# Kernel tuning notes

Measured on AMD Instinct MI355X. Metric: run time of the kernel, lower is better.

## Reference

```python
import jax, jax.numpy as jnp
import numpy as np

B, T, D = 2, 4096, 2048
H, K = 16, 128          # num_heads, head_dim (V == K)
P = H * K               # projection size
C = 64                  # chunk_size
CONV = 4                # conv_size
LAT = 128               # snapshot_latent_dim
CPS = 256 // C          # chunks_per_snapshot
EPS = 1e-6


def _silu(x):
    return x * jax.nn.sigmoid(x)


def _dwconv_silu(x, w):
    # causal depthwise conv1d: x (B,T,P), w (P,CONV)
    y = jax.lax.conv_general_dilated(
        x.transpose(0, 2, 1), w[:, None, :], (1,), [(w.shape[-1] - 1, 0)],
        feature_group_count=x.shape[-1], dimension_numbers=('NCH', 'OIH', 'NCH'))
    return _silu(y.transpose(0, 2, 1))


def _rmsnorm(x, w, eps=EPS):
    return x * jax.lax.rsqrt(jnp.mean(x * x, axis=-1, keepdims=True) + eps) * w


def _l2norm(x):
    return x * jax.lax.rsqrt(jnp.sum(x * x, axis=-1, keepdims=True) + 1e-12)


def setup_inputs() -> dict:
    key = jax.random.key(0)
    ks = jax.random.split(key, 20)
    sD, sK = D ** -0.5, K ** -0.5
    return {
        'x': jax.random.normal(ks[0], (B, T, D), jnp.float32),
        'Wq': jax.random.normal(ks[1], (P, D), jnp.float32) * sD,
        'Wk': jax.random.normal(ks[2], (P, D), jnp.float32) * sD,
        'Wv': jax.random.normal(ks[3], (P, D), jnp.float32) * sD,
        'conv_q': jax.random.normal(ks[4], (P, CONV), jnp.float32) * 0.5,
        'conv_k': jax.random.normal(ks[5], (P, CONV), jnp.float32) * 0.5,
        'conv_v': jax.random.normal(ks[6], (P, CONV), jnp.float32) * 0.5,
        'A_log': jnp.log(jax.random.uniform(ks[7], (H,), jnp.float32, 1.0, 8.0)),
        'dt_bias': jax.random.normal(ks[8], (P,), jnp.float32) * 0.1 - 3.0,
        'Wfa': jax.random.normal(ks[9], (K, D), jnp.float32) * sD,
        'Wfb': jax.random.normal(ks[10], (P, K), jnp.float32) * sK,
        'Wb': jax.random.normal(ks[11], (H, D), jnp.float32) * sD,
        'Wga': jax.random.normal(ks[12], (K, D), jnp.float32) * sD,
        'Wgb': jax.random.normal(ks[13], (P, K), jnp.float32) * sK,
        'bgb': jnp.zeros((P,), jnp.float32),
        'o_norm_w': jnp.ones((K,), jnp.float32),
        'Wo': jax.random.normal(ks[14], (D, P), jnp.float32) * (P ** -0.5),
        'snap_norm_w': jnp.ones((K * K,), jnp.float32),
        'snap_down': jax.random.normal(ks[15], (LAT, K * K), jnp.float32) * (K ** -1.0),
    }


def _forward(x, Wq, Wk, Wv, conv_q, conv_k, conv_v, A_log, dt_bias, Wfa, Wfb,
             Wb, Wga, Wgb, bgb, o_norm_w, Wo, snap_norm_w, snap_down):
    Bx, Tx, _ = x.shape
    Nc = Tx // C
    # projections + short causal conv + silu
    q = _dwconv_silu(x @ Wq.T, conv_q).reshape(Bx, Tx, H, K)
    k = _dwconv_silu(x @ Wk.T, conv_k).reshape(Bx, Tx, H, K)
    v = _dwconv_silu(x @ Wv.T, conv_v).reshape(Bx, Tx, H, K)
    # KDA gate: log forget gate per (t, h, k)
    g_raw = (x @ Wfa.T) @ Wfb.T                               # (B,T,P)
    log_g = (-jnp.exp(A_log))[None, None, :, None] * \
        jax.nn.softplus(g_raw + dt_bias).reshape(Bx, Tx, H, K)
    beta = jax.nn.sigmoid(x @ Wb.T)                           # (B,T,H)
    # qk l2-norm + scale
    q = _l2norm(q) * (K ** -0.5)
    k = _l2norm(k)
    # chunk: (B,T,H,K) -> (B,H,Nc,C,K)
    def ch(a):
        return a.reshape(Bx, Nc, C, H, -1).transpose(0, 3, 1, 2, 4)
    qc, kc, vc, gc = ch(q), ch(k), ch(v), ch(log_g)
    bc = beta.reshape(Bx, Nc, C, H).transpose(0, 3, 1, 2)     # (B,H,Nc,C)
    cum = jnp.maximum(jnp.cumsum(gc, axis=-2), -15.0)
    Wg = jnp.exp(cum)
    Wi = jnp.exp(-cum)
    u_mat = kc * Wi
    w_mat = kc * Wg
    q_tilde = qc * Wg
    be = bc[..., None]
    bw = be * w_mat
    bv = be * vc
    L = jnp.tril(jnp.einsum('bhnik,bhnjk->bhnij', bw, u_mat), -1)
    A_mat = L + jnp.eye(C, dtype=L.dtype)
    ev = jax.lax.linalg.triangular_solve(A_mat, bv, left_side=True, lower=True, unit_diagonal=True)
    ew = jax.lax.linalg.triangular_solve(A_mat, bw, left_side=True, lower=True, unit_diagonal=True)
    intra = jnp.tril(jnp.einsum('bhnik,bhnjk->bhnij', q_tilde, u_mat), 0)
    w_last = Wg[..., -1, :]                                   # (B,H,Nc,K)

    def body(S, inp):
        qt_n, um_n, ev_n, ew_n, ia_n, wl_n = inp
        delta = ev_n - ew_n @ S                               # (B,H,C,V)
        o_n = qt_n @ S + ia_n @ delta
        S_new = wl_n[..., None] * (S + jnp.einsum('bhck,bhcv->bhkv', um_n, delta))
        return S_new, (o_n, S_new)

    xs = tuple(jnp.moveaxis(a, 2, 0) for a in (q_tilde, u_mat, ev, ew, intra, w_last))
    S0 = jnp.zeros((Bx, H, K, K), jnp.float32)
    _, (o_chunks, S_all) = jax.lax.scan(body, S0, xs)
    out = o_chunks.transpose(1, 0, 3, 2, 4).reshape(Bx, Tx, H, K)
    # compressed snapshots every CPS chunks
    S_snap = S_all[CPS - 1::CPS]                              # (Ns,B,H,K,K)
    Ns = S_snap.shape[0]
    flat = S_snap.reshape(Ns, Bx, H, K * K)
    snaps = (_rmsnorm(flat, snap_norm_w) @ snap_down.T).transpose(1, 0, 2, 3)  # (B,Ns,H,LAT)
    # gated output norm + output projection
    gate = ((x @ Wga.T) @ Wgb.T + bgb).reshape(Bx, Tx, H, K)
    o = _rmsnorm(out, o_norm_w) * jax.nn.sigmoid(gate)
    y = o.reshape(Bx, Tx, P) @ Wo.T
    return y, snaps


def reference(x, Wq, Wk, Wv, conv_q, conv_k, conv_v, A_log, dt_bias, Wfa, Wfb,
              Wb, Wga, Wgb, bgb, o_norm_w, Wo, snap_norm_w, snap_down):
    return _forward(x, Wq, Wk, Wv, conv_q, conv_k, conv_v, A_log, dt_bias,
                    Wfa, Wfb, Wb, Wga, Wgb, bgb, o_norm_w, Wo,
                    snap_norm_w, snap_down)
```

## Files before the change

kernel.cpp:

```cpp
#include <hip/hip_runtime.h>

constexpr int Bc   = 2;
constexpr int Tc   = 4096;
constexpr int Dc   = 2048;
constexpr int Hc   = 16;
constexpr int Kc   = 128;
constexpr int Pc   = Hc * Kc;
constexpr int Cc   = 64;
constexpr int NCc  = Tc / Cc;
constexpr int Mc   = Bc * Tc;
constexpr int LATc = 128;

__device__ __forceinline__ float bf2f(unsigned short u) {
  unsigned int x = ((unsigned int)u) << 16;
  return __builtin_bit_cast(float, x);
}
__device__ __forceinline__ unsigned short f2bf(float f) {
  unsigned int x = __builtin_bit_cast(unsigned int, f);
  x += 0x7fffu + ((x >> 16) & 1u);
  return (unsigned short)(x >> 16);
}
__device__ __forceinline__ float4 ld4(const float* p) {
  return *reinterpret_cast<const float4*>(p);
}
__device__ __forceinline__ float4 ld4(const unsigned short* p) {
  ushort4 u = *reinterpret_cast<const ushort4*>(p);
  return make_float4(bf2f(u.x), bf2f(u.y), bf2f(u.z), bf2f(u.w));
}
__device__ __forceinline__ void st1(float* p, float v) { *p = v; }
__device__ __forceinline__ void st1(unsigned short* p, float v) { *p = f2bf(v); }

__device__ __forceinline__ float fsig(float x) {
  return __fdividef(1.f, 1.f + __expf(-x));
}
__device__ __forceinline__ float fsoftplus(float g) {
  return (g > 20.f) ? g : __logf(1.f + __expf(g));
}

typedef __attribute__((ext_vector_type(8))) short bf16x8;
typedef __attribute__((ext_vector_type(4))) float f32x4;

__device__ __forceinline__ int swzA(int row, int kbyte) { return row * 256 + (kbyte ^ ((row & 7) << 4)); }
__device__ __forceinline__ int swzB(int row, int kbyte) { return row * 128 + (kbyte ^ ((row & 7) << 4)); }
__device__ __forceinline__ bf16x8 ldsv8(const unsigned short* base, int byteoff) {
  return *reinterpret_cast<const bf16x8*>(reinterpret_cast<const char*>(base) + byteoff);
}
__device__ __forceinline__ void stsv16B(unsigned short* base, int byteoff, int4 v) {
  *reinterpret_cast<int4*>(reinterpret_cast<char*>(base) + byteoff) = v;
}
__device__ __forceinline__ void stsv8B(unsigned short* base, int byteoff, uint2 v) {
  *reinterpret_cast<uint2*>(reinterpret_cast<char*>(base) + byteoff) = v;
}
__device__ __forceinline__ unsigned short lds16(const unsigned short* base, int byteoff) {
  return *reinterpret_cast<const unsigned short*>(reinterpret_cast<const char*>(base) + byteoff);
}

__device__ __forceinline__ int xcd_swz(int id, int nwg) {
  if ((nwg & 7) != 0 || nwg < 16) return id;
  return (id & 7) * (nwg >> 3) + (id >> 3);
}

__global__ void cast_f32_bf16(const float* __restrict__ in, unsigned short* __restrict__ out,
                              int n) {
  int i = (blockIdx.x * 256 + threadIdx.x) * 4;
  if (i < n) {
    float4 v = ld4(in + i);
    ushort4 o;
    o.x = f2bf(v.x); o.y = f2bf(v.y); o.z = f2bf(v.z); o.w = f2bf(v.w);
    *reinterpret_cast<ushort4*>(out + i) = o;
  }
}

__device__ __forceinline__ void gload_lds16(const unsigned short* g, unsigned short* l) {
  __builtin_amdgcn_global_load_lds(
      (const __attribute__((address_space(1))) void*)g,
      (__attribute__((address_space(3))) void*)l, 16, 0, 0);
}

__device__ __forceinline__ void tile_map(int& m0, int& n0) {
  int id = blockIdx.y * gridDim.x + blockIdx.x;
  id = xcd_swz(id, gridDim.x * gridDim.y);
  const int bpg = gridDim.y << 3;
  int grp = id / bpg, rem = id % bpg;
  m0 = ((grp << 3) + (rem & 7)) * 128;
  n0 = (rem >> 3) * 128;
}

template <typename OT>
__global__ __launch_bounds__(256) void gemm_nt_mfma(const unsigned short* __restrict__ A,
                                                    const unsigned short* __restrict__ Bm,
                                                    OT* __restrict__ Out,
                                                    int Ndim, int Kd) {
  __shared__ __align__(16) unsigned short As[128 * 32];
  __shared__ __align__(16) unsigned short Bs[128 * 32];
  int m0, n0;
  tile_map(m0, n0);
  const int tid = threadIdx.x;
  const int wave = tid >> 6;
  const int lane = tid & 63;
  const int wr = wave >> 1, wc = wave & 1;
  const int l15 = lane & 15, l4 = lane >> 4;
  const int kxor = (l4 ^ ((l15 >> 1) & 3)) << 3;
  f32x4 acc[4][4] = {};

  for (int k0 = 0; k0 < Kd; k0 += 32) {
#pragma unroll
    for (int i = 0; i < 2; ++i) {
      int slot = (wave * 2 + i) * 64 + lane;
      int r = slot >> 2;
      int kg = (slot & 3) ^ ((r >> 1) & 3);
      gload_lds16(&A[(size_t)(m0 + r) * Kd + k0 + kg * 8], &As[(wave * 2 + i) * 512]);
      gload_lds16(&Bm[(size_t)(n0 + r) * Kd + k0 + kg * 8], &Bs[(wave * 2 + i) * 512]);
    }
    __syncthreads();
    bf16x8 af[4], bfr[4];
#pragma unroll
    for (int m = 0; m < 4; ++m)
      af[m] = *reinterpret_cast<const bf16x8*>(&As[(wr * 64 + m * 16 + l15) * 32 + kxor]);
#pragma unroll
    for (int n = 0; n < 4; ++n)
      bfr[n] = *reinterpret_cast<const bf16x8*>(&Bs[(wc * 64 + n * 16 + l15) * 32 + kxor]);
#pragma unroll
    for (int m = 0; m < 4; ++m)
#pragma unroll
      for (int n = 0; n < 4; ++n)
        acc[m][n] = __builtin_amdgcn_mfma_f32_16x16x32_bf16(af[m], bfr[n], acc[m][n], 0, 0, 0);
    __syncthreads();
  }
#pragma unroll
  for (int m = 0; m < 4; ++m)
#pragma unroll
    for (int n = 0; n < 4; ++n)
#pragma unroll
      for (int r = 0; r < 4; ++r) {
        int row = m0 + wr * 64 + m * 16 + l4 * 4 + r;
        int col = n0 + wc * 64 + n * 16 + l15;
        st1(&Out[(size_t)row * Ndim + col], acc[m][n][r]);
      }
}

__global__ __launch_bounds__(256) void gemm_nt_mfma_qkv(const unsigned short* __restrict__ A,
                                                        const unsigned short* __restrict__ Bm,
                                                        unsigned short* __restrict__ Out,
                                                        int Kd) {
  __shared__ __align__(16) unsigned short As[128 * 32];
  __shared__ __align__(16) unsigned short Bs[128 * 32];
  int m0, n0;
  tile_map(m0, n0);
  const int tid = threadIdx.x;
  const int wave = tid >> 6;
  const int lane = tid & 63;
  const int wr = wave >> 1, wc = wave & 1;
  const int l15 = lane & 15, l4 = lane >> 4;
  const int kxor = (l4 ^ ((l15 >> 1) & 3)) << 3;
  f32x4 acc[4][4] = {};

  for (int k0 = 0; k0 < Kd; k0 += 32) {
#pragma unroll
    for (int i = 0; i < 2; ++i) {
      int slot = (wave * 2 + i) * 64 + lane;
      int r = slot >> 2;
      int kg = (slot & 3) ^ ((r >> 1) & 3);
      gload_lds16(&A[(size_t)(m0 + r) * Kd + k0 + kg * 8], &As[(wave * 2 + i) * 512]);
      gload_lds16(&Bm[(size_t)(n0 + r) * Kd + k0 + kg * 8], &Bs[(wave * 2 + i) * 512]);
    }
    __syncthreads();
    bf16x8 af[4], bfr[4];
#pragma unroll
    for (int m = 0; m < 4; ++m)
      af[m] = *reinterpret_cast<const bf16x8*>(&As[(wr * 64 + m * 16 + l15) * 32 + kxor]);
#pragma unroll
    for (int n = 0; n < 4; ++n)
      bfr[n] = *reinterpret_cast<const bf16x8*>(&Bs[(wc * 64 + n * 16 + l15) * 32 + kxor]);
#pragma unroll
    for (int m = 0; m < 4; ++m)
#pragma unroll
      for (int n = 0; n < 4; ++n)
        acc[m][n] = __builtin_amdgcn_mfma_f32_16x16x32_bf16(af[m], bfr[n], acc[m][n], 0, 0, 0);
    __syncthreads();
  }
  unsigned short* dst = Out + (size_t)(n0 >> 11) * ((size_t)Mc * 2048);
  const int cbase = n0 & 2047;
#pragma unroll
  for (int m = 0; m < 4; ++m)
#pragma unroll
    for (int n = 0; n < 4; ++n)
#pragma unroll
      for (int r = 0; r < 4; ++r) {
        int row = m0 + wr * 64 + m * 16 + l4 * 4 + r;
        int col = cbase + wc * 64 + n * 16 + l15;
        dst[(size_t)row * 2048 + col] = f2bf(acc[m][n][r]);
      }
}

__global__ __launch_bounds__(256) void gemm_nt_mfma_sk(const unsigned short* __restrict__ A,
                                                       const unsigned short* __restrict__ Bm,
                                                       float* __restrict__ Part,
                                                       int Ndim, int Kd, int kslice, int Mtot) {
  __shared__ __align__(16) unsigned short As[128 * 32];
  __shared__ __align__(16) unsigned short Bs[128 * 32];
  const int m0 = blockIdx.x * 128;
  const int n0 = blockIdx.y * 128;
  const int kz = blockIdx.z * kslice;
  const int tid = threadIdx.x;
  const int wave = tid >> 6;
  const int lane = tid & 63;
  const int wr = wave >> 1, wc = wave & 1;
  const int l15 = lane & 15, l4 = lane >> 4;
  const int kxor = (l4 ^ ((l15 >> 1) & 3)) << 3;
  f32x4 acc[4][4] = {};

  for (int k0 = kz; k0 < kz + kslice; k0 += 32) {
#pragma unroll
    for (int i = 0; i < 2; ++i) {
      int slot = (wave * 2 + i) * 64 + lane;
      int r = slot >> 2;
      int kg = (slot & 3) ^ ((r >> 1) & 3);
      gload_lds16(&A[(size_t)(m0 + r) * Kd + k0 + kg * 8], &As[(wave * 2 + i) * 512]);
      gload_lds16(&Bm[(size_t)(n0 + r) * Kd + k0 + kg * 8], &Bs[(wave * 2 + i) * 512]);
    }
    __syncthreads();
    bf16x8 af[4], bfr[4];
#pragma unroll
    for (int m = 0; m < 4; ++m)
      af[m] = *reinterpret_cast<const bf16x8*>(&As[(wr * 64 + m * 16 + l15) * 32 + kxor]);
#pragma unroll
    for (int n = 0; n < 4; ++n)
      bfr[n] = *reinterpret_cast<const bf16x8*>(&Bs[(wc * 64 + n * 16 + l15) * 32 + kxor]);
#pragma unroll
    for (int m = 0; m < 4; ++m)
#pragma unroll
      for (int n = 0; n < 4; ++n)
        acc[m][n] = __builtin_amdgcn_mfma_f32_16x16x32_bf16(af[m], bfr[n], acc[m][n], 0, 0, 0);
    __syncthreads();
  }
  float* out = Part + (size_t)blockIdx.z * Mtot * Ndim;
#pragma unroll
  for (int m = 0; m < 4; ++m)
#pragma unroll
    for (int n = 0; n < 4; ++n)
#pragma unroll
      for (int r = 0; r < 4; ++r) {
        int row = m0 + wr * 64 + m * 16 + l4 * 4 + r;
        int col = n0 + wc * 64 + n * 16 + l15;
        out[(size_t)row * Ndim + col] = acc[m][n][r];
      }
}

__global__ __launch_bounds__(256) void chunk_prep(
    const unsigned short* __restrict__ q_lin, const unsigned short* __restrict__ k_lin,
    const unsigned short* __restrict__ v_lin, const unsigned short* __restrict__ g_raw,
    const float* __restrict__ beta_lin, const float* __restrict__ conv_q,
    const float* __restrict__ conv_k, const float* __restrict__ conv_v,
    const float* __restrict__ A_log, const float* __restrict__ dt_bias,
    unsigned short* __restrict__ qt, unsigned short* __restrict__ u_,
    unsigned short* __restrict__ bv, unsigned short* __restrict__ bw,
    float* __restrict__ wlast) {
  const int wave = threadIdx.x >> 6, lane = threadIdx.x & 63;
  const int cid = blockIdx.x * 4 + wave;
  const int n = cid & 63;
  const int h = (cid >> 6) & 15;
  const int b = cid >> 10;
  const int k0 = 2 * lane;
  const int p = h * Kc + k0;
  float cq[2][4], ck[2][4], cv[2][4];
#pragma unroll
  for (int s = 0; s < 2; ++s)
#pragma unroll
    for (int j = 0; j < 4; ++j) {
      cq[s][j] = conv_q[(p + s) * 4 + j];
      ck[s][j] = conv_k[(p + s) * 4 + j];
      cv[s][j] = conv_v[(p + s) * 4 + j];
    }
  const float aneg = -__expf(A_log[h]);
  const float db0 = dt_bias[p], db1 = dt_bias[p + 1];
  float cum0 = 0.f, cum1 = 0.f;
  const int t0 = n * Cc;
  float wq[2][3] = {}, wk[2][3] = {}, wv[2][3] = {};
#pragma unroll
  for (int d = 0; d < 3; ++d) {
    int ts = t0 - 3 + d;
    if (ts >= 0) {
      size_t o = ((size_t)(b * Tc + ts)) * Pc + p;
      ushort2 q2 = *(const ushort2*)(q_lin + o);
      ushort2 k2 = *(const ushort2*)(k_lin + o);
      ushort2 v2 = *(const ushort2*)(v_lin + o);
      wq[0][d] = bf2f(q2.x); wq[1][d] = bf2f(q2.y);
      wk[0][d] = bf2f(k2.x); wk[1][d] = bf2f(k2.y);
      wv[0][d] = bf2f(v2.x); wv[1][d] = bf2f(v2.y);
    }
  }
  for (int c = 0; c < Cc; ++c) {
    const int t = t0 + c;
    size_t off = ((size_t)(b * Tc + t)) * Pc + p;
    ushort2 q2 = *(const ushort2*)(q_lin + off);
    ushort2 k2 = *(const ushort2*)(k_lin + off);
    ushort2 v2 = *(const ushort2*)(v_lin + off);
    ushort2 g2 = *(const ushort2*)(g_raw + off);
    float nq[2] = {bf2f(q2.x), bf2f(q2.y)};
    float nk[2] = {bf2f(k2.x), bf2f(k2.y)};
    float nv[2] = {bf2f(v2.x), bf2f(v2.y)};
    float qv[2], kv[2], vv[2];
#pragma unroll
    for (int s = 0; s < 2; ++s) {
      qv[s] = cq[s][0] * wq[s][0] + cq[s][1] * wq[s][1] + cq[s][2] * wq[s][2] + cq[s][3] * nq[s];
      kv[s] = ck[s][0] * wk[s][0] + ck[s][1] * wk[s][1] + ck[s][2] * wk[s][2] + ck[s][3] * nk[s];
      vv[s] = cv[s][0] * wv[s][0] + cv[s][1] * wv[s][1] + cv[s][2] * wv[s][2] + cv[s][3] * nv[s];
      wq[s][0] = wq[s][1]; wq[s][1] = wq[s][2]; wq[s][2] = nq[s];
      wk[s][0] = wk[s][1]; wk[s][1] = wk[s][2]; wk[s][2] = nk[s];
      wv[s][0] = wv[s][1]; wv[s][1] = wv[s][2]; wv[s][2] = nv[s];
      qv[s] = qv[s] * fsig(qv[s]);
      kv[s] = kv[s] * fsig(kv[s]);
      vv[s] = vv[s] * fsig(vv[s]);
    }
    float a = qv[0] * qv[0] + qv[1] * qv[1];
    float bb = kv[0] * kv[0] + kv[1] * kv[1];
#pragma unroll
    for (int off2 = 32; off2 > 0; off2 >>= 1) {
      a += __shfl_xor(a, off2, 64);
      bb += __shfl_xor(bb, off2, 64);
    }
    float rq = rsqrtf(a + 1e-12f) * 0.08838834764831845f;
    float rk = rsqrtf(bb + 1e-12f);
    float g0 = bf2f(g2.x) + db0, g1 = bf2f(g2.y) + db1;
    cum0 += aneg * fsoftplus(g0);
    cum1 += aneg * fsoftplus(g1);
    float cc0 = fmaxf(cum0, -15.f), cc1 = fmaxf(cum1, -15.f);
    float Wg0 = __expf(cc0), Wg1 = __expf(cc1);
    float Wi0 = __fdividef(1.f, Wg0), Wi1 = __fdividef(1.f, Wg1);
    float beta = fsig(beta_lin[((size_t)(b * Tc + t)) * 128 + h]);
    size_t idx = ((size_t)cid * Cc + c) * Kc + k0;
    ushort2 o1, o2, o3, o4;
    o1.x = f2bf(qv[0] * rq * Wg0); o1.y = f2bf(qv[1] * rq * Wg1);
    o2.x = f2bf(kv[0] * rk * Wi0); o2.y = f2bf(kv[1] * rk * Wi1);
    o3.x = f2bf(beta * kv[0] * rk * Wg0); o3.y = f2bf(beta * kv[1] * rk * Wg1);
    o4.x = f2bf(beta * vv[0]); o4.y = f2bf(beta * vv[1]);
    *(ushort2*)(qt + idx) = o1;
    *(ushort2*)(u_ + idx) = o2;
    *(ushort2*)(bw + idx) = o3;
    *(ushort2*)(bv + idx) = o4;
    if (c == Cc - 1) {
      wlast[(size_t)cid * Kc + k0] = Wg0;
      wlast[(size_t)cid * Kc + k0 + 1] = Wg1;
    }
  }
}

__global__ __launch_bounds__(256) void chunk_solve_mfma(
    const unsigned short* __restrict__ qt, unsigned short* __restrict__ u_,
    unsigned short* __restrict__ evb,
    unsigned short* __restrict__ ewb,
    unsigned short* __restrict__ intra_out) {
  const int blk = blockIdx.x;
  const size_t base = (size_t)blk * (Cc * Kc);
  const size_t ibase = (size_t)blk * (Cc * Cc);
  const int tid = threadIdx.x, wave = tid >> 6, lane = tid & 63;
  const int l15 = lane & 15, l4 = lane >> 4;

  __shared__ __align__(16) char lds[65536];
  unsigned short* uS   = (unsigned short*)(lds);
  unsigned short* qtS  = (unsigned short*)(lds + 16384);
  unsigned short* bwS  = (unsigned short*)(lds + 32768);
  unsigned short* NLrm = (unsigned short*)(lds + 49152);
  unsigned short* NLT  = (unsigned short*)(lds + 57344);
  unsigned short* Trm  = (unsigned short*)(lds);
  unsigned short* TT   = (unsigned short*)(lds + 8192);
  unsigned short* Prm  = (unsigned short*)(lds + 16384);
  unsigned short* PT   = (unsigned short*)(lds + 24576);
  unsigned short* bvT  = (unsigned short*)(lds + 32768);
  unsigned short* bwT  = (unsigned short*)(lds + 49152);

#pragma unroll
  for (int i = 0; i < 4; ++i) {
    int cid = tid + i * 256;
    int r = cid >> 4, c8 = (cid & 15) * 8, cb2 = (cid & 15) * 16;
    int4 vu = *(const int4*)(u_ + base + (size_t)r * 128 + c8);
    int4 vb = *(const int4*)(ewb + base + (size_t)r * 128 + c8);
    int4 vq = *(const int4*)(qt + base + (size_t)r * 128 + c8);
    stsv16B(uS, swzA(r, cb2), vu);
    stsv16B(bwS, swzA(r, cb2), vb);
    stsv16B(qtS, swzA(r, cb2), vq);
  }
  __syncthreads();

  const int arow = 16 * wave + l15;
  bf16x8 aBw[4], aQt[4];
#pragma unroll
  for (int ks = 0; ks < 4; ++ks) {
    aBw[ks] = ldsv8(bwS, swzA(arow, 16 * l4 + 64 * ks));
    aQt[ks] = ldsv8(qtS, swzA(arow, 16 * l4 + 64 * ks));
  }
  f32x4 Lc[4], Ic[4];
#pragma unroll
  for (int nt = 0; nt < 4; ++nt) {
    f32x4 a = {}, bq = {};
#pragma unroll
    for (int ks = 0; ks < 4; ++ks) {
      bf16x8 bu = ldsv8(uS, swzA(16 * nt + l15, 16 * l4 + 64 * ks));
      a = __builtin_amdgcn_mfma_f32_16x16x32_bf16(aBw[ks], bu, a, 0, 0, 0);
      bq = __builtin_amdgcn_mfma_f32_16x16x32_bf16(aQt[ks], bu, bq, 0, 0, 0);
    }
    Lc[nt] = a; Ic[nt] = bq;
  }
#pragma unroll
  for (int nt = 0; nt < 4; ++nt)
#pragma unroll
    for (int r = 0; r < 4; ++r) {
      int row = 16 * wave + 4 * l4 + r, col = 16 * nt + l15;
      intra_out[ibase + (size_t)row * 64 + col] = f2bf((col <= row) ? Ic[nt][r] : 0.f);
    }

#pragma unroll
  for (int i = 0; i < 4; ++i) {
    int w2 = tid + i * 256;
    int k = w2 >> 3, cg = w2 & 7;
    unsigned short tmp[8];
#pragma unroll
    for (int j = 0; j < 8; ++j) {
      int c = cg + 8 * j;
      tmp[j] = lds16(uS, swzA(c, 2 * k));
    }
#pragma unroll
    for (int j = 0; j < 8; ++j)
      u_[base + (size_t)k * 64 + cg + 8 * j] = tmp[j];
  }
  __syncthreads();

  f32x4 Tf[4];
#pragma unroll
  for (int nt = 0; nt < 4; ++nt)
#pragma unroll
    for (int r = 0; r < 4; ++r) {
      int row = 16 * wave + 4 * l4 + r, col = 16 * nt + l15;
      float nl = (col < row) ? -Lc[nt][r] : 0.f;
      unsigned short nb = f2bf(nl);
      *reinterpret_cast<unsigned short*>((char*)NLrm + swzB(row, col * 2)) = nb;
      *reinterpret_cast<unsigned short*>((char*)NLT + swzB(col, row * 2)) = nb;
      float t0 = nl + ((row == col) ? 1.f : 0.f);
      Tf[nt][r] = t0;
      unsigned short tb = f2bf(t0);
      *reinterpret_cast<unsigned short*>((char*)Trm + swzB(row, col * 2)) = tb;
      *reinterpret_cast<unsigned short*>((char*)TT + swzB(col, row * 2)) = tb;
    }
  __syncthreads();

  bf16x8 aN[2];
#pragma unroll
  for (int ks = 0; ks < 2; ++ks) aN[ks] = ldsv8(NLrm, swzB(arow, 16 * l4 + 64 * ks));
  f32x4 Pf[4];
#pragma unroll
  for (int nt = 0; nt < 4; ++nt) {
    f32x4 acc = {};
#pragma unroll
    for (int ks = 0; ks < 2; ++ks)
      acc = __builtin_amdgcn_mfma_f32_16x16x32_bf16(aN[ks], ldsv8(NLT, swzB(16 * nt + l15, 16 * l4 + 64 * ks)), acc, 0, 0, 0);
    Pf[nt] = acc;
  }
  int4 rv[4], rw[4];
#pragma unroll
  for (int i = 0; i < 4; ++i) {
    int cid = tid + i * 256;
    int r = cid >> 4, c8 = (cid & 15) * 8;
    rv[i] = *(const int4*)(evb + base + (size_t)r * 128 + c8);
    rw[i] = *(const int4*)(ewb + base + (size_t)r * 128 + c8);
  }
#pragma unroll
  for (int nt = 0; nt < 4; ++nt)
#pragma unroll
    for (int r = 0; r < 4; ++r) {
      int row = 16 * wave + 4 * l4 + r, col = 16 * nt + l15;
      unsigned short pb = f2bf(Pf[nt][r]);
      *reinterpret_cast<unsigned short*>((char*)Prm + swzB(row, col * 2)) = pb;
      *reinterpret_cast<unsigned short*>((char*)PT + swzB(col, row * 2)) = pb;
    }
  __syncthreads();

  for (int it = 0; it < 5; ++it) {
    bf16x8 aP[2];
#pragma unroll
    for (int ks = 0; ks < 2; ++ks) aP[ks] = ldsv8(Prm, swzB(arow, 16 * l4 + 64 * ks));
    f32x4 Tn[4], Pn[4];
#pragma unroll
    for (int nt = 0; nt < 4; ++nt) {
      f32x4 acc = Tf[nt];
#pragma unroll
      for (int ks = 0; ks < 2; ++ks)
        acc = __builtin_amdgcn_mfma_f32_16x16x32_bf16(aP[ks], ldsv8(TT, swzB(16 * nt + l15, 16 * l4 + 64 * ks)), acc, 0, 0, 0);
      Tn[nt] = acc;
    }
    if (it < 4) {
#pragma unroll
      for (int nt = 0; nt < 4; ++nt) {
        f32x4 acc = {};
#pragma unroll
        for (int ks = 0; ks < 2; ++ks)
          acc = __builtin_amdgcn_mfma_f32_16x16x32_bf16(aP[ks], ldsv8(PT, swzB(16 * nt + l15, 16 * l4 + 64 * ks)), acc, 0, 0, 0);
        Pn[nt] = acc;
      }
    }
    __syncthreads();
#pragma unroll
    for (int nt = 0; nt < 4; ++nt)
#pragma unroll
      for (int r = 0; r < 4; ++r) {
        int row = 16 * wave + 4 * l4 + r, col = 16 * nt + l15;
        unsigned short tb = f2bf(Tn[nt][r]);
        *reinterpret_cast<unsigned short*>((char*)Trm + swzB(row, col * 2)) = tb;
        *reinterpret_cast<unsigned short*>((char*)TT + swzB(col, row * 2)) = tb;
        if (it < 4) {
          unsigned short pb = f2bf(Pn[nt][r]);
          *reinterpret_cast<unsigned short*>((char*)Prm + swzB(row, col * 2)) = pb;
          *reinterpret_cast<unsigned short*>((char*)PT + swzB(col, row * 2)) = pb;
        }
      }
#pragma unroll
    for (int nt = 0; nt < 4; ++nt) Tf[nt] = Tn[nt];
    __syncthreads();
  }

#pragma unroll
  for (int i = 0; i < 4; ++i) {
    int cid = tid + i * 256;
    int r = cid >> 4;
    const unsigned short* pv = reinterpret_cast<const unsigned short*>(&rv[i]);
    const unsigned short* pw = reinterpret_cast<const unsigned short*>(&rw[i]);
#pragma unroll
    for (int j = 0; j < 8; ++j) {
      int v = (cid & 15) * 8 + j;
      *reinterpret_cast<unsigned short*>((char*)bvT + swzB(v, r * 2)) = pv[j];
      *reinterpret_cast<unsigned short*>((char*)bwT + swzB(v, r * 2)) = pw[j];
    }
  }
  __syncthreads();

  bf16x8 aT[2];
#pragma unroll
  for (int ks = 0; ks < 2; ++ks) aT[ks] = ldsv8(Trm, swzB(arow, 16 * l4 + 64 * ks));
#pragma unroll
  for (int nt = 0; nt < 8; ++nt) {
    f32x4 e = {}, w2 = {};
#pragma unroll
    for (int ks = 0; ks < 2; ++ks) {
      e = __builtin_amdgcn_mfma_f32_16x16x32_bf16(aT[ks], ldsv8(bvT, swzB(16 * nt + l15, 16 * l4 + 64 * ks)), e, 0, 0, 0);
      w2 = __builtin_amdgcn_mfma_f32_16x16x32_bf16(aT[ks], ldsv8(bwT, swzB(16 * nt + l15, 16 * l4 + 64 * ks)), w2, 0, 0, 0);
    }
#pragma unroll
    for (int r = 0; r < 4; ++r) {
      int row = 16 * wave + 4 * l4 + r, col = 16 * nt + l15;
      evb[base + (size_t)row * 128 + col] = f2bf(e[r]);
      ewb[base + (size_t)row * 128 + col] = f2bf(w2[r]);
    }
  }
}

__global__ __launch_bounds__(512) void scan_mfma(
    const unsigned short* __restrict__ qt, const unsigned short* __restrict__ uT,
    const unsigned short* __restrict__ evb, const unsigned short* __restrict__ ewb,
    const unsigned short* __restrict__ intra, const float* __restrict__ wlast,
    unsigned short* __restrict__ attn_o, unsigned short* __restrict__ snapb) {
  const int blk = blockIdx.x;
  const int bh = blk >> 1, vh = blk & 1;
  const int b = bh >> 4, h = bh & 15;
  const int v0 = vh * 64;
  const int tid = threadIdx.x, wave = tid >> 6, lane = tid & 63;
  const int l15 = lane & 15, l4 = lane >> 4;
  __shared__ __align__(16) unsigned short ewS[8192];
  __shared__ __align__(16) unsigned short qtS[8192];
  __shared__ __align__(16) unsigned short uTS[8192];
  __shared__ __align__(16) unsigned short iaS[4096];
  __shared__ __align__(16) unsigned short evS[4096];
  __shared__ __align__(16) unsigned short sBT[8192];
  __shared__ __align__(16) unsigned short dBT[4096];

  f32x4 S[4] = {};
  {
    int4 z = {0, 0, 0, 0};
    stsv16B(sBT, tid * 32, z);
    stsv16B(sBT, tid * 32 + 16, z);
  }

  const int sr = tid >> 3;
  const int sk0 = (tid & 7) * 16;
  const int sc0 = (tid & 7) * 8;
  const int tk = tid >> 3;
  const int wloff = 16 * wave + 4 * l4;
  int4 rEw0, rEw1, rQt0, rQt1, rEv, rUT0, rUT1, rIa;
  float4 rWlN, rWlC;

#define STAGE_LOAD(CB, IB, NN)                                                    \
  rEw0 = *(const int4*)(ewb + (CB) + sr * 128 + sk0);                             \
  rEw1 = *(const int4*)(ewb + (CB) + sr * 128 + sk0 + 8);                         \
  rQt0 = *(const int4*)(qt + (CB) + sr * 128 + sk0);                              \
  rQt1 = *(const int4*)(qt + (CB) + sr * 128 + sk0 + 8);                          \
  rEv = *(const int4*)(evb + (CB) + sr * 128 + v0 + sc0);                         \
  rUT0 = *(const int4*)(uT + (CB) + (size_t)tk * 64 + sc0);                       \
  rUT1 = *(const int4*)(uT + (CB) + (size_t)(tk + 64) * 64 + sc0);                \
  rIa = *(const int4*)(intra + (IB) + sr * 64 + sc0);                             \
  rWlN = ld4(wlast + ((size_t)bh * 64 + (NN)) * 128 + wloff);

#define STAGE_WRITE()                                                             \
  stsv16B(ewS, swzA(sr, sk0 * 2), rEw0);                                          \
  stsv16B(ewS, swzA(sr, sk0 * 2 + 16), rEw1);                                     \
  stsv16B(qtS, swzA(sr, sk0 * 2), rQt0);                                          \
  stsv16B(qtS, swzA(sr, sk0 * 2 + 16), rQt1);                                     \
  stsv16B(evS, swzB(sr, sc0 * 2), rEv);                                           \
  stsv16B(iaS, swzB(sr, sc0 * 2), rIa);                                           \
  stsv16B(uTS, swzB(tk, sc0 * 2), rUT0);                                          \
  stsv16B(uTS, swzB(tk + 64, sc0 * 2), rUT1);

  {
    const size_t cb0 = (size_t)bh * 64 * 8192;
    const size_t ib0 = (size_t)bh * 64 * 4096;
    STAGE_LOAD(cb0, ib0, 0);
    STAGE_WRITE();
    rWlC = rWlN;
  }
  __syncthreads();

  const int m = wave & 3, ntb = (wave >> 2) * 2;
  const int arow = 16 * m + l15;
  const int krow = 16 * wave + l15;

  for (int n = 0; n < NCc; ++n) {
    const size_t cb = ((size_t)bh * 64 + n) * 8192;
    const size_t ib = ((size_t)bh * 64 + n) * 4096;
    if (n < 63) { STAGE_LOAD(cb + 8192, ib + 4096, n + 1); }
    bf16x8 aEw[4];
#pragma unroll
    for (int ks = 0; ks < 4; ++ks) aEw[ks] = ldsv8(ewS, swzA(arow, 16 * l4 + 64 * ks));
#pragma unroll
    for (int i = 0; i < 2; ++i) {
      int vl = 16 * (ntb + i) + l15;
      f32x4 p = {};
#pragma unroll
      for (int ks = 0; ks < 4; ++ks)
        p = __builtin_amdgcn_mfma_f32_16x16x32_bf16(aEw[ks], ldsv8(sBT, swzA(vl, 16 * l4 + 64 * ks)), p, 0, 0, 0);
      float d[4];
#pragma unroll
      for (int r = 0; r < 4; ++r) {
        int c = 16 * m + 4 * l4 + r;
        d[r] = bf2f(lds16(evS, swzB(c, 2 * vl))) - p[r];
      }
      uint2 pk;
      pk.x = (unsigned)f2bf(d[0]) | ((unsigned)f2bf(d[1]) << 16);
      pk.y = (unsigned)f2bf(d[2]) | ((unsigned)f2bf(d[3]) << 16);
      stsv8B(dBT, swzB(vl, (16 * m + 4 * l4) * 2), pk);
    }
    __syncthreads();
    bf16x8 aQt[4], aIa[2], aU[2];
#pragma unroll
    for (int ks = 0; ks < 4; ++ks) aQt[ks] = ldsv8(qtS, swzA(arow, 16 * l4 + 64 * ks));
#pragma unroll
    for (int ks = 0; ks < 2; ++ks) aIa[ks] = ldsv8(iaS, swzB(arow, 16 * l4 + 64 * ks));
#pragma unroll
    for (int ks = 0; ks < 2; ++ks) aU[ks] = ldsv8(uTS, swzB(krow, 16 * l4 + 64 * ks));
#pragma unroll
    for (int i = 0; i < 2; ++i) {
      int vl = 16 * (ntb + i) + l15;
      f32x4 o = {};
#pragma unroll
      for (int ks = 0; ks < 4; ++ks)
        o = __builtin_amdgcn_mfma_f32_16x16x32_bf16(aQt[ks], ldsv8(sBT, swzA(vl, 16 * l4 + 64 * ks)), o, 0, 0, 0);
#pragma unroll
      for (int ks = 0; ks < 2; ++ks)
        o = __builtin_amdgcn_mfma_f32_16x16x32_bf16(aIa[ks], ldsv8(dBT, swzB(vl, 16 * l4 + 64 * ks)), o, 0, 0, 0);
#pragma unroll
      for (int r = 0; r < 4; ++r) {
        int c = 16 * m + 4 * l4 + r;
        int t = n * 64 + c;
        attn_o[((size_t)(b * Tc + t) * Hc + h) * Kc + v0 + vl] = f2bf(o[r]);
      }
    }
    float wlv[4] = {rWlC.x, rWlC.y, rWlC.z, rWlC.w};
#pragma unroll
    for (int nt4 = 0; nt4 < 4; ++nt4) {
      int vl = 16 * nt4 + l15;
      f32x4 U = {};
#pragma unroll
      for (int ks = 0; ks < 2; ++ks)
        U = __builtin_amdgcn_mfma_f32_16x16x32_bf16(aU[ks], ldsv8(dBT, swzB(vl, 16 * l4 + 64 * ks)), U, 0, 0, 0);
#pragma unroll
      for (int r = 0; r < 4; ++r) S[nt4][r] = wlv[r] * (S[nt4][r] + U[r]);
    }
    __syncthreads();
#pragma unroll
    for (int nt4 = 0; nt4 < 4; ++nt4) {
      int vl = 16 * nt4 + l15;
      uint2 pk;
      pk.x = (unsigned)f2bf(S[nt4][0]) | ((unsigned)f2bf(S[nt4][1]) << 16);
      pk.y = (unsigned)f2bf(S[nt4][2]) | ((unsigned)f2bf(S[nt4][3]) << 16);
      stsv8B(sBT, swzA(vl, (16 * wave + 4 * l4) * 2), pk);
    }
    if (n < 63) { STAGE_WRITE(); rWlC = rWlN; }
    if ((n & 3) == 3) {
      int ns = n >> 2;
      size_t sb = (size_t)((ns * Bc + b) * Hc + h) * 16384;
#pragma unroll
      for (int nt4 = 0; nt4 < 4; ++nt4)
#pragma unroll
        for (int r = 0; r < 4; ++r) {
          int k = 16 * wave + 4 * l4 + r;
          snapb[sb + (size_t)k * 128 + v0 + 16 * nt4 + l15] = f2bf(S[nt4][r]);
        }
    }
    __syncthreads();
  }
#undef STAGE_LOAD
#undef STAGE_WRITE
}

__global__ void sdw_mul_bf16(const float* __restrict__ snap_down, const float* __restrict__ w,
                             unsigned short* __restrict__ sdwb) {
  int i = (blockIdx.x * 256 + threadIdx.x) * 4;
  float4 v = ld4(snap_down + i);
  int k = i & 16383;
  float4 ww = ld4(w + k);
  ushort4 o;
  o.x = f2bf(v.x * ww.x); o.y = f2bf(v.y * ww.y); o.z = f2bf(v.z * ww.z); o.w = f2bf(v.w * ww.w);
  *reinterpret_cast<ushort4*>(sdwb + i) = o;
}

__global__ __launch_bounds__(256) void snap_scale_kernel(const unsigned short* __restrict__ snapb,
                                                         float* __restrict__ scale) {
  int r = blockIdx.x;
  const unsigned short* row = snapb + (size_t)r * 16384;
  float s = 0.f;
  for (int ii = threadIdx.x * 4; ii < 16384; ii += 1024) {
    float4 x = ld4(row + ii);
    s += x.x * x.x + x.y * x.y + x.z * x.z + x.w * x.w;
  }
#pragma unroll
  for (int off = 32; off > 0; off >>= 1) s += __shfl_down(s, off, 64);
  __shared__ float red[4];
  if ((threadIdx.x & 63) == 0) red[threadIdx.x >> 6] = s;
  __syncthreads();
  if (threadIdx.x == 0) {
    float tot = red[0] + red[1] + red[2] + red[3];
    scale[r] = rsqrtf(tot * (1.f / 16384.f) + 1e-6f);
  }
}

__global__ void snap_reduce_scatter(const float* __restrict__ part,
                                    const float* __restrict__ scale,
                                    float* __restrict__ outp) {
  int idx = blockIdx.x * 256 + threadIdx.x;
  int l = idx & 127;
  int hh = (idx >> 7) & 15;
  int ns = (idx >> 11) & 15;
  int bb = idx >> 15;
  int r = (ns * Bc + bb) * Hc + hh;
  float s = 0.f;
#pragma unroll
  for (int z = 0; z < 16; ++z) s += part[(size_t)z * 65536 + r * 128 + l];
  outp[idx] = s * scale[r];
}

__global__ __launch_bounds__(256) void out_norm_gate(unsigned short* __restrict__ attn_io,
                                                     const unsigned short* __restrict__ gate_raw,
                                                     const float* __restrict__ bgb,
                                                     const float* __restrict__ o_norm_w) {
  const int wave = threadIdx.x >> 6, lane = threadIdx.x & 63;
  const int blk = blockIdx.x * 4 + wave;
  const int h = blk & 15;
  const size_t row = (size_t)(blk >> 4);
  const size_t base = (size_t)blk * Kc;
  ushort2 xv = *reinterpret_cast<const ushort2*>(attn_io + base + 2 * lane);
  float x0 = bf2f(xv.x), x1 = bf2f(xv.y);
  float ss = x0 * x0 + x1 * x1;
#pragma unroll
  for (int off = 32; off > 0; off >>= 1) ss += __shfl_xor(ss, off, 64);
  float inv = rsqrtf(ss * (1.f / 128.f) + 1e-6f);
  const int p0 = h * Kc + 2 * lane;
  ushort2 gv = *reinterpret_cast<const ushort2*>(gate_raw + row * Pc + p0);
  float g0 = bf2f(gv.x) + bgb[p0];
  float g1 = bf2f(gv.y) + bgb[p0 + 1];
  float o0 = x0 * inv * o_norm_w[2 * lane] * fsig(g0);
  float o1 = x1 * inv * o_norm_w[2 * lane + 1] * fsig(g1);
  ushort2 ov; ov.x = f2bf(o0); ov.y = f2bf(o1);
  *reinterpret_cast<ushort2*>(attn_io + base + 2 * lane) = ov;
}

extern "C" void kernel_launch(void* const* d_in, const int* in_sizes, int n_in,
                              void* d_out, int out_size, void* d_ws, size_t ws_size,
                              hipStream_t stream) {
  (void)in_sizes; (void)n_in;
  const float* x        = (const float*)d_in[0];
  const float* Wq       = (const float*)d_in[1];
  const float* Wk       = (const float*)d_in[2];
  const float* Wv       = (const float*)d_in[3];
  const float* conv_q   = (const float*)d_in[4];
  const float* conv_k   = (const float*)d_in[5];
  const float* conv_v   = (const float*)d_in[6];
  const float* A_log    = (const float*)d_in[7];
  const float* dt_bias  = (const float*)d_in[8];
  const float* Wfa      = (const float*)d_in[9];
  const float* Wfb      = (const float*)d_in[10];
  const float* Wb       = (const float*)d_in[11];
  const float* Wga      = (const float*)d_in[12];
  const float* Wgb      = (const float*)d_in[13];
  const float* bgb      = (const float*)d_in[14];
  const float* o_norm_w = (const float*)d_in[15];
  const float* Wo       = (const float*)d_in[16];
  const float* snap_nw  = (const float*)d_in[17];
  const float* snap_down= (const float*)d_in[18];

  const size_t MP2 = (size_t)Mc * Pc * 2;
  const size_t NEED = 6 * MP2
                    + 2 * (size_t)Mc * Kc * 4
                    + (size_t)Mc * Hc * 4
                    + (size_t)Bc * Hc * NCc * Kc * 4;
  if (ws_size < NEED + 4096) {
    hipMemsetAsync(d_out, 0, (size_t)out_size * 4, stream);
    return;
  }
  char* w = (char*)d_ws;
  auto alloc = [&](size_t bytes) {
    char* r = w;
    w += (bytes + 255) & ~(size_t)255;
    return r;
  };
  unsigned short* q_lin = (unsigned short*)alloc(MP2);
  unsigned short* k_lin = (unsigned short*)alloc(MP2);
  unsigned short* v_lin = (unsigned short*)alloc(MP2);
  unsigned short* g_raw = (unsigned short*)alloc(MP2);
  unsigned short* evb   = (unsigned short*)alloc(MP2);
  unsigned short* ewb   = (unsigned short*)alloc(MP2);
  float* fa    = (float*)alloc((size_t)Mc * Kc * 4);
  float* ga    = (float*)alloc((size_t)Mc * Kc * 4);
  float* betab = (float*)alloc((size_t)Mc * Hc * 4);
  float* wlast = (float*)alloc((size_t)Bc * Hc * NCc * Kc * 4);
  (void)betab;

  unsigned short* qt = (unsigned short*)d_out;
  unsigned short* u_ = (unsigned short*)((char*)d_out + MP2);

  unsigned short* xb    = evb;
  unsigned short* Wqb   = ewb;
  unsigned short* Wkb   = ewb + 4194304;
  unsigned short* Wvb   = ewb + 8388608;
  unsigned short* Wfab  = ewb + 12582912;
  unsigned short* Wgab  = ewb + 12845056;
  unsigned short* Wfbb  = ewb + 13107200;
  unsigned short* Wbp   = ewb + 13369344;
  unsigned short* fab   = (unsigned short*)fa;
  unsigned short* gab   = (unsigned short*)ga;
  float* betap          = fa;

  unsigned short* intra = q_lin;
  unsigned short* Wob   = q_lin + 8388608;
  unsigned short* Wgbb  = q_lin + 12582912;
  unsigned short* attn  = k_lin;
  unsigned short* gate_raw = g_raw;
  unsigned short* snapb = v_lin;
  unsigned short* sdwb  = v_lin + (size_t)512 * 16384;
  float* partial   = (float*)ewb;
  float* snapscale = (float*)(ewb + 4400000);

  float* y = (float*)d_out;
  float* snaps_out = (float*)d_out + (size_t)Bc * Tc * Dc;

  cast_f32_bf16<<<16384, 256, 0, stream>>>(x, xb, Mc * Dc);
  cast_f32_bf16<<<4096, 256, 0, stream>>>(Wq, Wqb, Pc * Dc);
  cast_f32_bf16<<<4096, 256, 0, stream>>>(Wk, Wkb, Pc * Dc);
  cast_f32_bf16<<<4096, 256, 0, stream>>>(Wv, Wvb, Pc * Dc);
  cast_f32_bf16<<<256, 256, 0, stream>>>(Wfa, Wfab, Kc * Dc);
  cast_f32_bf16<<<256, 256, 0, stream>>>(Wga, Wgab, Kc * Dc);
  cast_f32_bf16<<<256, 256, 0, stream>>>(Wfb, Wfbb, Pc * Kc);
  hipMemsetAsync(Wbp, 0, (size_t)128 * 2048 * 2, stream);
  cast_f32_bf16<<<32, 256, 0, stream>>>(Wb, Wbp, Hc * Dc);

  gemm_nt_mfma_qkv<<<dim3(64, 48), 256, 0, stream>>>(xb, Wqb, q_lin, Dc);
  gemm_nt_mfma<unsigned short><<<dim3(64, 1), 256, 0, stream>>>(xb, Wfab, fab, Kc, Dc);
  gemm_nt_mfma<unsigned short><<<dim3(64, 1), 256, 0, stream>>>(xb, Wgab, gab, Kc, Dc);
  gemm_nt_mfma<unsigned short><<<dim3(64, 16), 256, 0, stream>>>(fab, Wfbb, g_raw, Pc, Kc);
  gemm_nt_mfma<float><<<dim3(64, 1), 256, 0, stream>>>(xb, Wbp, betap, 128, Dc);

  chunk_prep<<<Bc * Hc * NCc / 4, 256, 0, stream>>>(q_lin, k_lin, v_lin, g_raw, betap, conv_q,
                                                    conv_k, conv_v, A_log, dt_bias, qt, u_, evb,
                                                    ewb, wlast);

  cast_f32_bf16<<<4096, 256, 0, stream>>>(Wo, Wob, Dc * Pc);
  cast_f32_bf16<<<256, 256, 0, stream>>>(Wgb, Wgbb, Pc * Kc);

  chunk_solve_mfma<<<Bc * Hc * NCc, 256, 0, stream>>>(qt, u_, evb, ewb, intra);

  gemm_nt_mfma<unsigned short><<<dim3(64, 16), 256, 0, stream>>>(gab, Wgbb, gate_raw, Pc, Kc);

  scan_mfma<<<Bc * Hc * 2, 512, 0, stream>>>(qt, u_, evb, ewb, intra, wlast, attn, snapb);

  sdw_mul_bf16<<<2048, 256, 0, stream>>>(snap_down, snap_nw, sdwb);
  snap_scale_kernel<<<512, 256, 0, stream>>>(snapb, snapscale);
  gemm_nt_mfma_sk<<<dim3(4, 1, 16), 256, 0, stream>>>(snapb, sdwb, partial, 128, 16384, 1024, 512);
  snap_reduce_scatter<<<256, 256, 0, stream>>>(partial, snapscale, snaps_out);

  out_norm_gate<<<Mc * Hc / 4, 256, 0, stream>>>(attn, gate_raw, bgb, o_norm_w);
  gemm_nt_mfma<float><<<dim3(64, 16), 256, 0, stream>>>(attn, Wob, y, Dc, Pc);
}
```

Before: 985.5 us.

## Split scan across four value slices and fuse small x-projection GEMMs

The sequential chunk scan now splits the value dimension into four 32-wide slices instead of two 64-wide halves. This doubles the number of workgroups to 128 and halves the per-block state and LDS, with an XCD-aware block remap. Separately, the three small projections of x (Wfa, Wga, Wb) are merged into one GEMM launch by placing their bf16 weights contiguously, and beta is now stored in bf16. The trade-off is that each scan block redundantly reloads the shared chunk operands (qt, ew, u, intra), and beta loses precision.

```diff
diff --git a/kernel.cpp b/kernel.cpp
--- a/kernel.cpp
+++ b/kernel.cpp
@@ -42,6 +42,7 @@
 
 __device__ __forceinline__ int swzA(int row, int kbyte) { return row * 256 + (kbyte ^ ((row & 7) << 4)); }
 __device__ __forceinline__ int swzB(int row, int kbyte) { return row * 128 + (kbyte ^ ((row & 7) << 4)); }
+__device__ __forceinline__ int swzC(int row, int kbyte) { return row * 64 + (kbyte ^ (((row >> 2) & 3) << 4)); }
 __device__ __forceinline__ bf16x8 ldsv8(const unsigned short* base, int byteoff) {
   return *reinterpret_cast<const bf16x8*>(reinterpret_cast<const char*>(base) + byteoff);
 }
@@ -193,6 +194,61 @@
       }
 }
 
+__global__ __launch_bounds__(256) void gemm_nt_mfma_fgb(const unsigned short* __restrict__ A,
+                                                        const unsigned short* __restrict__ Bm,
+                                                        unsigned short* __restrict__ fab,
+                                                        unsigned short* __restrict__ gab,
+                                                        unsigned short* __restrict__ betabb,
+                                                        int Kd) {
+  __shared__ __align__(16) unsigned short As[128 * 32];
+  __shared__ __align__(16) unsigned short Bs[128 * 32];
+  int m0, n0;
+  tile_map(m0, n0);
+  const int tid = threadIdx.x;
+  const int wave = tid >> 6;
+  const int lane = tid & 63;
+  const int wr = wave >> 1, wc = wave & 1;
+  const int l15 = lane & 15, l4 = lane >> 4;
+  const int kxor = (l4 ^ ((l15 >> 1) & 3)) << 3;
+  f32x4 acc[4][4] = {};
+
+  for (int k0 = 0; k0 < Kd; k0 += 32) {
+#pragma unroll
+    for (int i = 0; i < 2; ++i) {
+      int slot = (wave * 2 + i) * 64 + lane;
+      int r = slot >> 2;
+      int kg = (slot & 3) ^ ((r >> 1) & 3);
+      gload_lds16(&A[(size_t)(m0 + r) * Kd + k0 + kg * 8], &As[(wave * 2 + i) * 512]);
+      gload_lds16(&Bm[(size_t)(n0 + r) * Kd + k0 + kg * 8], &Bs[(wave * 2 + i) * 512]);
+    }
+    __syncthreads();
+    bf16x8 af[4], bfr[4];
+#pragma unroll
+    for (int m = 0; m < 4; ++m)
+      af[m] = *reinterpret_cast<const bf16x8*>(&As[(wr * 64 + m * 16 + l15) * 32 + kxor]);
+#pragma unroll
+    for (int n = 0; n < 4; ++n)
+      bfr[n] = *reinterpret_cast<const bf16x8*>(&Bs[(wc * 64 + n * 16 + l15) * 32 + kxor]);
+#pragma unroll
+    for (int m = 0; m < 4; ++m)
+#pragma unroll
+      for (int n = 0; n < 4; ++n)
+        acc[m][n] = __builtin_amdgcn_mfma_f32_16x16x32_bf16(af[m], bfr[n], acc[m][n], 0, 0, 0);
+    __syncthreads();
+  }
+  unsigned short* dst = (n0 == 0) ? fab : ((n0 == 128) ? gab : betabb);
+#pragma unroll
+  for (int m = 0; m < 4; ++m)
+#pragma unroll
+    for (int n = 0; n < 4; ++n)
+#pragma unroll
+      for (int r = 0; r < 4; ++r) {
+        int row = m0 + wr * 64 + m * 16 + l4 * 4 + r;
+        int lc = wc * 64 + n * 16 + l15;
+        dst[(size_t)row * 128 + lc] = f2bf(acc[m][n][r]);
+      }
+}
+
 __global__ __launch_bounds__(256) void gemm_nt_mfma_sk(const unsigned short* __restrict__ A,
                                                        const unsigned short* __restrict__ Bm,
                                                        float* __restrict__ Part,
@@ -250,7 +306,7 @@
 __global__ __launch_bounds__(256) void chunk_prep(
     const unsigned short* __restrict__ q_lin, const unsigned short* __restrict__ k_lin,
     const unsigned short* __restrict__ v_lin, const unsigned short* __restrict__ g_raw,
-    const float* __restrict__ beta_lin, const float* __restrict__ conv_q,
+    const unsigned short* __restrict__ beta16, const float* __restrict__ conv_q,
     const float* __restrict__ conv_k, const float* __restrict__ conv_v,
     const float* __restrict__ A_log, const float* __restrict__ dt_bias,
     unsigned short* __restrict__ qt, unsigned short* __restrict__ u_,
@@ -328,7 +384,7 @@
     float cc0 = fmaxf(cum0, -15.f), cc1 = fmaxf(cum1, -15.f);
     float Wg0 = __expf(cc0), Wg1 = __expf(cc1);
     float Wi0 = __fdividef(1.f, Wg0), Wi1 = __fdividef(1.f, Wg1);
-    float beta = fsig(beta_lin[((size_t)(b * Tc + t)) * 128 + h]);
+    float beta = fsig(bf2f(beta16[((size_t)(b * Tc + t)) * 128 + h]));
     size_t idx = ((size_t)cid * Cc + c) * Kc + k0;
     ushort2 o1, o2, o3, o4;
     o1.x = f2bf(qv[0] * rq * Wg0); o1.y = f2bf(qv[1] * rq * Wg1);
@@ -558,33 +614,34 @@
     const unsigned short* __restrict__ evb, const unsigned short* __restrict__ ewb,
     const unsigned short* __restrict__ intra, const float* __restrict__ wlast,
     unsigned short* __restrict__ attn_o, unsigned short* __restrict__ snapb) {
-  const int blk = blockIdx.x;
-  const int bh = blk >> 1, vh = blk & 1;
+  const int id = xcd_swz(blockIdx.x, 128);
+  const int bh = id >> 2, vs = id & 3;
   const int b = bh >> 4, h = bh & 15;
-  const int v0 = vh * 64;
+  const int v0 = vs * 32;
   const int tid = threadIdx.x, wave = tid >> 6, lane = tid & 63;
   const int l15 = lane & 15, l4 = lane >> 4;
   __shared__ __align__(16) unsigned short ewS[8192];
   __shared__ __align__(16) unsigned short qtS[8192];
   __shared__ __align__(16) unsigned short uTS[8192];
   __shared__ __align__(16) unsigned short iaS[4096];
-  __shared__ __align__(16) unsigned short evS[4096];
-  __shared__ __align__(16) unsigned short sBT[8192];
-  __shared__ __align__(16) unsigned short dBT[4096];
-
-  f32x4 S[4] = {};
+  __shared__ __align__(16) unsigned short evS[2048];
+  __shared__ __align__(16) unsigned short sBT[4096];
+  __shared__ __align__(16) unsigned short dBT[2048];
+
+  f32x4 S[2] = {};
   {
     int4 z = {0, 0, 0, 0};
-    stsv16B(sBT, tid * 32, z);
-    stsv16B(sBT, tid * 32 + 16, z);
+    stsv16B(sBT, tid * 16, z);
   }
 
   const int sr = tid >> 3;
   const int sk0 = (tid & 7) * 16;
   const int sc0 = (tid & 7) * 8;
+  const int evc = (tid & 7) * 4;
   const int tk = tid >> 3;
   const int wloff = 16 * wave + 4 * l4;
-  int4 rEw0, rEw1, rQt0, rQt1, rEv, rUT0, rUT1, rIa;
+  int4 rEw0, rEw1, rQt0, rQt1, rUT0, rUT1, rIa;
+  uint2 rEv;
   float4 rWlN, rWlC;
 
 #define STAGE_LOAD(CB, IB, NN)                                                    \
@@ -592,7 +649,7 @@
   rEw1 = *(const int4*)(ewb + (CB) + sr * 128 + sk0 + 8);                         \
   rQt0 = *(const int4*)(qt + (CB) + sr * 128 + sk0);                              \
   rQt1 = *(const int4*)(qt + (CB) + sr * 128 + sk0 + 8);                          \
-  rEv = *(const int4*)(evb + (CB) + sr * 128 + v0 + sc0);                         \
+  rEv = *(const uint2*)(evb + (CB) + sr * 128 + v0 + evc);                        \
   rUT0 = *(const int4*)(uT + (CB) + (size_t)tk * 64 + sc0);                       \
   rUT1 = *(const int4*)(uT + (CB) + (size_t)(tk + 64) * 64 + sc0);                \
   rIa = *(const int4*)(intra + (IB) + sr * 64 + sc0);                             \
@@ -603,7 +660,7 @@
   stsv16B(ewS, swzA(sr, sk0 * 2 + 16), rEw1);                                     \
   stsv16B(qtS, swzA(sr, sk0 * 2), rQt0);                                          \
   stsv16B(qtS, swzA(sr, sk0 * 2 + 16), rQt1);                                     \
-  stsv16B(evS, swzB(sr, sc0 * 2), rEv);                                           \
+  stsv8B(evS, swzC(sr, evc * 2), rEv);                                            \
   stsv16B(iaS, swzB(sr, sc0 * 2), rIa);                                           \
   stsv16B(uTS, swzB(tk, sc0 * 2), rUT0);                                          \
   stsv16B(uTS, swzB(tk + 64, sc0 * 2), rUT1);
@@ -617,9 +674,10 @@
   }
   __syncthreads();
 
-  const int m = wave & 3, ntb = (wave >> 2) * 2;
+  const int m = wave & 3, vg = wave >> 2;
   const int arow = 16 * m + l15;
   const int krow = 16 * wave + l15;
+  const int vl = 16 * vg + l15;
 
   for (int n = 0; n < NCc; ++n) {
     const size_t cb = ((size_t)bh * 64 + n) * 8192;
@@ -628,9 +686,7 @@
     bf16x8 aEw[4];
 #pragma unroll
     for (int ks = 0; ks < 4; ++ks) aEw[ks] = ldsv8(ewS, swzA(arow, 16 * l4 + 64 * ks));
-#pragma unroll
-    for (int i = 0; i < 2; ++i) {
-      int vl = 16 * (ntb + i) + l15;
+    {
       f32x4 p = {};
 #pragma unroll
       for (int ks = 0; ks < 4; ++ks)
@@ -639,7 +695,7 @@
 #pragma unroll
       for (int r = 0; r < 4; ++r) {
         int c = 16 * m + 4 * l4 + r;
-        d[r] = bf2f(lds16(evS, swzB(c, 2 * vl))) - p[r];
+        d[r] = bf2f(lds16(evS, swzC(c, 2 * vl))) - p[r];
       }
       uint2 pk;
       pk.x = (unsigned)f2bf(d[0]) | ((unsigned)f2bf(d[1]) << 16);
@@ -654,9 +710,7 @@
     for (int ks = 0; ks < 2; ++ks) aIa[ks] = ldsv8(iaS, swzB(arow, 16 * l4 + 64 * ks));
 #pragma unroll
     for (int ks = 0; ks < 2; ++ks) aU[ks] = ldsv8(uTS, swzB(krow, 16 * l4 + 64 * ks));
-#pragma unroll
-    for (int i = 0; i < 2; ++i) {
-      int vl = 16 * (ntb + i) + l15;
+    {
       f32x4 o = {};
 #pragma unroll
       for (int ks = 0; ks < 4; ++ks)
@@ -673,34 +727,34 @@
     }
     float wlv[4] = {rWlC.x, rWlC.y, rWlC.z, rWlC.w};
 #pragma unroll
-    for (int nt4 = 0; nt4 < 4; ++nt4) {
-      int vl = 16 * nt4 + l15;
+    for (int vt2 = 0; vt2 < 2; ++vt2) {
+      int vl2 = 16 * vt2 + l15;
       f32x4 U = {};
 #pragma unroll
       for (int ks = 0; ks < 2; ++ks)
-        U = __builtin_amdgcn_mfma_f32_16x16x32_bf16(aU[ks], ldsv8(dBT, swzB(vl, 16 * l4 + 64 * ks)), U, 0, 0, 0);
-#pragma unroll
-      for (int r = 0; r < 4; ++r) S[nt4][r] = wlv[r] * (S[nt4][r] + U[r]);
-    }
-    __syncthreads();
-#pragma unroll
-    for (int nt4 = 0; nt4 < 4; ++nt4) {
-      int vl = 16 * nt4 + l15;
+        U = __builtin_amdgcn_mfma_f32_16x16x32_bf16(aU[ks], ldsv8(dBT, swzB(vl2, 16 * l4 + 64 * ks)), U, 0, 0, 0);
+#pragma unroll
+      for (int r = 0; r < 4; ++r) S[vt2][r] = wlv[r] * (S[vt2][r] + U[r]);
+    }
+    __syncthreads();
+#pragma unroll
+    for (int vt2 = 0; vt2 < 2; ++vt2) {
+      int vl2 = 16 * vt2 + l15;
       uint2 pk;
-      pk.x = (unsigned)f2bf(S[nt4][0]) | ((unsigned)f2bf(S[nt4][1]) << 16);
-      pk.y = (unsigned)f2bf(S[nt4][2]) | ((unsigned)f2bf(S[nt4][3]) << 16);
-      stsv8B(sBT, swzA(vl, (16 * wave + 4 * l4) * 2), pk);
+      pk.x = (unsigned)f2bf(S[vt2][0]) | ((unsigned)f2bf(S[vt2][1]) << 16);
+      pk.y = (unsigned)f2bf(S[vt2][2]) | ((unsigned)f2bf(S[vt2][3]) << 16);
+      stsv8B(sBT, swzA(vl2, (16 * wave + 4 * l4) * 2), pk);
     }
     if (n < 63) { STAGE_WRITE(); rWlC = rWlN; }
     if ((n & 3) == 3) {
       int ns = n >> 2;
       size_t sb = (size_t)((ns * Bc + b) * Hc + h) * 16384;
 #pragma unroll
-      for (int nt4 = 0; nt4 < 4; ++nt4)
+      for (int vt2 = 0; vt2 < 2; ++vt2)
 #pragma unroll
         for (int r = 0; r < 4; ++r) {
           int k = 16 * wave + 4 * l4 + r;
-          snapb[sb + (size_t)k * 128 + v0 + 16 * nt4 + l15] = f2bf(S[nt4][r]);
+          snapb[sb + (size_t)k * 128 + v0 + 16 * vt2 + l15] = f2bf(S[vt2][r]);
         }
     }
     __syncthreads();
@@ -840,11 +894,11 @@
   unsigned short* Wvb   = ewb + 8388608;
   unsigned short* Wfab  = ewb + 12582912;
   unsigned short* Wgab  = ewb + 12845056;
-  unsigned short* Wfbb  = ewb + 13107200;
-  unsigned short* Wbp   = ewb + 13369344;
+  unsigned short* Wbp   = ewb + 13107200;
+  unsigned short* Wfbb  = ewb + 13369344;
   unsigned short* fab   = (unsigned short*)fa;
+  unsigned short* betabb= (unsigned short*)fa + 1048576;
   unsigned short* gab   = (unsigned short*)ga;
-  float* betap          = fa;
 
   unsigned short* intra = q_lin;
   unsigned short* Wob   = q_lin + 8388608;
@@ -865,17 +919,15 @@
   cast_f32_bf16<<<4096, 256, 0, stream>>>(Wv, Wvb, Pc * Dc);
   cast_f32_bf16<<<256, 256, 0, stream>>>(Wfa, Wfab, Kc * Dc);
   cast_f32_bf16<<<256, 256, 0, stream>>>(Wga, Wgab, Kc * Dc);
-  cast_f32_bf16<<<256, 256, 0, stream>>>(Wfb, Wfbb, Pc * Kc);
   hipMemsetAsync(Wbp, 0, (size_t)128 * 2048 * 2, stream);
   cast_f32_bf16<<<32, 256, 0, stream>>>(Wb, Wbp, Hc * Dc);
+  cast_f32_bf16<<<256, 256, 0, stream>>>(Wfb, Wfbb, Pc * Kc);
 
   gemm_nt_mfma_qkv<<<dim3(64, 48), 256, 0, stream>>>(xb, Wqb, q_lin, Dc);
-  gemm_nt_mfma<unsigned short><<<dim3(64, 1), 256, 0, stream>>>(xb, Wfab, fab, Kc, Dc);
-  gemm_nt_mfma<unsigned short><<<dim3(64, 1), 256, 0, stream>>>(xb, Wgab, gab, Kc, Dc);
+  gemm_nt_mfma_fgb<<<dim3(64, 3), 256, 0, stream>>>(xb, Wfab, fab, gab, betabb, Dc);
   gemm_nt_mfma<unsigned short><<<dim3(64, 16), 256, 0, stream>>>(fab, Wfbb, g_raw, Pc, Kc);
-  gemm_nt_mfma<float><<<dim3(64, 1), 256, 0, stream>>>(xb, Wbp, betap, 128, Dc);
-
-  chunk_prep<<<Bc * Hc * NCc / 4, 256, 0, stream>>>(q_lin, k_lin, v_lin, g_raw, betap, conv_q,
+
+  chunk_prep<<<Bc * Hc * NCc / 4, 256, 0, stream>>>(q_lin, k_lin, v_lin, g_raw, betabb, conv_q,
                                                     conv_k, conv_v, A_log, dt_bias, qt, u_, evb,
                                                     ewb, wlast);
 
@@ -886,7 +938,7 @@
 
   gemm_nt_mfma<unsigned short><<<dim3(64, 16), 256, 0, stream>>>(gab, Wgbb, gate_raw, Pc, Kc);
 
-  scan_mfma<<<Bc * Hc * 2, 512, 0, stream>>>(qt, u_, evb, ewb, intra, wlast, attn, snapb);
+  scan_mfma<<<Bc * Hc * 4, 512, 0, stream>>>(qt, u_, evb, ewb, intra, wlast, attn, snapb);
 
   sdw_mul_bf16<<<2048, 256, 0, stream>>>(snap_down, snap_nw, sdwb);
   snap_scale_kernel<<<512, 256, 0, stream>>>(snapb, snapscale);
```

Result: faster. 858.8 us, median of 3 (-12.9%).
